# Kernel tuning notes

Hardware: AMD Instinct MI355X
Metric: run time of the kernel (lower is better)

The kernel has to match this reference:

```python
import jax, jax.numpy as jnp
import numpy as np

NUM_HEADS = 16

def setup_inputs() -> dict:
    key = jax.random.key(0)
    ks = jax.random.split(key, 9)
    B, S, D = 8, 1024, 1024
    scale = 1.0 / np.sqrt(D)
    return {
        "query": jax.random.normal(ks[0], (B, S, D), jnp.float32),
        "key": jax.random.normal(ks[1], (B, S, D), jnp.float32),
        "value": jax.random.normal(ks[2], (B, S, D), jnp.float32),
        "Wq": jax.random.normal(ks[3], (D, D), jnp.float32) * scale,
        "bq": jnp.zeros((D,), jnp.float32),
        "Wk": jax.random.normal(ks[4], (D, D), jnp.float32) * scale,
        "bk": jnp.zeros((D,), jnp.float32),
        "Wv": jax.random.normal(ks[5], (D, D), jnp.float32) * scale,
        "bv": jnp.zeros((D,), jnp.float32),
    }

def reference(query, key, value, Wq, bq, Wk, bk, Wv, bv):
    B, S, D = query.shape
    H = NUM_HEADS
    hd = D // H
    def proj(x, W, b):
        # [B, S, D] -> [B, H, S, hd]  (nn.Linear uses x @ W.T + b)
        return (x @ W.T + b).reshape(B, -1, H, hd).transpose(0, 2, 1, 3)
    q = proj(query, Wq, bq)
    k = proj(key, Wk, bk)
    v = proj(value, Wv, bv)
    scores = jnp.einsum('bhqd,bhkd->bhqk', q, k) / (hd ** 0.5)
    w = jax.nn.softmax(scores, axis=-1)
    # relu(tanh(.)) on non-negative softmax probs == tanh, but keep faithful
    w = jax.nn.relu(jnp.tanh(w))
    attn = jnp.einsum('bhqk,bhkd->bhqd', w, v)  # [B, H, Sq, hd]
    attn_output = attn.transpose(0, 2, 1, 3).reshape(B, -1, D)
    attn_output_weights = jnp.mean(w, axis=1)  # [B, Sq, Sk]
    return attn_output, attn_output_weights
```

## Files before the change

### kernel.cpp

```cpp
#include <hip/hip_runtime.h>
#include <hip/hip_bf16.h>

using bf16x8 = __attribute__((ext_vector_type(8))) short;
using f32x4  = __attribute__((ext_vector_type(4))) float;
typedef unsigned short u16;

__device__ __forceinline__ u16 f2bf(float f) {
  unsigned int u = __float_as_uint(f);
  u += 0x7FFFu + ((u >> 16) & 1u);
  return (u16)(u >> 16);
}

__device__ __forceinline__ u16 f2bf_fast(float f) {
  return (u16)((__float_as_uint(f) + 0x8000u) >> 16);
}

__device__ __forceinline__ float bf2f(u16 b) {
  return __uint_as_float(((unsigned int)b) << 16);
}

__device__ __forceinline__ f32x4 mfma16(bf16x8 a, bf16x8 b, f32x4 c) {
  return __builtin_amdgcn_mfma_f32_16x16x32_bf16(a, b, c, 0, 0, 0);
}

__device__ __forceinline__ float tanh2(float p) {
  float x2 = p * p;
  return p * fmaf(x2, -0.33333333f, 1.0f);
}

#define GLL16(gp, lp) __builtin_amdgcn_global_load_lds( \
    (const __attribute__((address_space(1))) unsigned*)(gp), \
    (__attribute__((address_space(3))) unsigned*)(lp), 16, 0, 0)

__global__ __launch_bounds__(256) void cvtX_kernel(
    const float* __restrict__ x0, const float* __restrict__ x1,
    const float* __restrict__ x2, u16* __restrict__ d0,
    u16* __restrict__ d1, u16* __restrict__ d2) {
  const float* src = (blockIdx.y == 0) ? x0 : (blockIdx.y == 1) ? x1 : x2;
  u16* dst = (blockIdx.y == 0) ? d0 : (blockIdx.y == 1) ? d1 : d2;
  const int i = (blockIdx.x * 256 + threadIdx.x) * 8;
  float4 v0 = *reinterpret_cast<const float4*>(src + i);
  float4 v1 = *reinterpret_cast<const float4*>(src + i + 4);
  u16 o[8] = {f2bf(v0.x), f2bf(v0.y), f2bf(v0.z), f2bf(v0.w),
              f2bf(v1.x), f2bf(v1.y), f2bf(v1.z), f2bf(v1.w)};
  *reinterpret_cast<int4*>(dst + i) = *reinterpret_cast<int4*>(o);
}

__global__ __launch_bounds__(256) void cvtW_kernel(
    const float* __restrict__ w0, const float* __restrict__ w1,
    const float* __restrict__ w2, u16* __restrict__ dst) {
  const float* src = (blockIdx.y == 0) ? w0 : (blockIdx.y == 1) ? w1 : w2;
  u16* d = dst + (size_t)blockIdx.y * 1048576;
  const int i = (blockIdx.x * 256 + threadIdx.x) * 8;
  float4 v0 = *reinterpret_cast<const float4*>(src + i);
  float4 v1 = *reinterpret_cast<const float4*>(src + i + 4);
  u16 o[8] = {f2bf(v0.x), f2bf(v0.y), f2bf(v0.z), f2bf(v0.w),
              f2bf(v1.x), f2bf(v1.y), f2bf(v1.z), f2bf(v1.w)};
  *reinterpret_cast<int4*>(d + i) = *reinterpret_cast<int4*>(o);
}

__global__ __launch_bounds__(256) void proj_kernel(
    const u16* __restrict__ Xq, const u16* __restrict__ Xk,
    const u16* __restrict__ Xv, const u16* __restrict__ Wbf,
    const float* __restrict__ Bq, const float* __restrict__ Bk,
    const float* __restrict__ Bv,
    u16* __restrict__ Yq, u16* __restrict__ Yk, u16* __restrict__ Yv)
{
  const int mat = blockIdx.z;
  const u16* X  = (mat == 0) ? Xq : (mat == 1) ? Xk : Xv;
  const u16* W  = Wbf + (size_t)mat * 1048576;
  const float* Bi = (mat == 0) ? Bq : (mat == 1) ? Bk : Bv;
  u16* Y = (mat == 0) ? Yq : (mat == 1) ? Yk : Yv;
  const float scale = (mat == 0) ? 0.125f : 1.0f;

  __shared__ u16 As[2][128][32];
  __shared__ u16 Bs[2][128][32];

  const int tid  = threadIdx.x;
  const int lane = tid & 63;
  const int w    = tid >> 6;
  const int m0 = blockIdx.x * 128;
  const int n0 = blockIdx.y * 128;
  const int wm = (w >> 1) * 64;
  const int wn = (w & 1) * 64;
  const int fr = lane & 15;
  const int fg = lane >> 4;

  const int srow = lane >> 2;
  const int scol = (lane & 3) * 8;
  const u16* agp = X + (size_t)(m0 + w*32 + srow) * 1024 + scol;
  const u16* bgp = W + (size_t)(n0 + w*32 + srow) * 1024 + scol;

  f32x4 zero = {0.f, 0.f, 0.f, 0.f};
  f32x4 acc[4][4];
#pragma unroll
  for (int i = 0; i < 4; i++)
#pragma unroll
    for (int j = 0; j < 4; j++) acc[i][j] = zero;

#define STAGE(buf, kk)                                            \
  do {                                                            \
    GLL16(agp + (kk),            &As[buf][w*32     ][0]);         \
    GLL16(agp + (kk) + 16*1024,  &As[buf][w*32 + 16][0]);         \
    GLL16(bgp + (kk),            &Bs[buf][w*32     ][0]);         \
    GLL16(bgp + (kk) + 16*1024,  &Bs[buf][w*32 + 16][0]);         \
  } while (0)

  STAGE(0, 0);
  __syncthreads();

  int cur = 0;
  for (int kt = 0; kt < 32; kt++) {
    if (kt < 31) STAGE(cur ^ 1, (kt + 1) * 32);

    bf16x8 af[4], bff[4];
#pragma unroll
    for (int i = 0; i < 4; i++) {
      af[i]  = *reinterpret_cast<const bf16x8*>(&As[cur][wm + i*16 + fr][fg*8]);
      bff[i] = *reinterpret_cast<const bf16x8*>(&Bs[cur][wn + i*16 + fr][fg*8]);
    }
#pragma unroll
    for (int i = 0; i < 4; i++)
#pragma unroll
      for (int j = 0; j < 4; j++)
        acc[i][j] = mfma16(af[i], bff[j], acc[i][j]);

    __syncthreads();
    cur ^= 1;
  }
#undef STAGE

#pragma unroll
  for (int j = 0; j < 4; j++) {
    const int n = n0 + wn + j*16 + fr;
    const float bias = Bi[n];
#pragma unroll
    for (int i = 0; i < 4; i++) {
      const int mbase = m0 + wm + i*16 + fg*4;
      if (mat == 2) {
        u16 pk[4];
#pragma unroll
        for (int r = 0; r < 4; r++) pk[r] = f2bf((acc[i][j][r] + bias) * scale);
        const int bidx = mbase >> 10;
        const int s = mbase & 1023;
        *reinterpret_cast<uint2*>(&Y[((size_t)(bidx * 1024 + n)) * 1024 + s]) =
            *reinterpret_cast<uint2*>(pk);
      } else {
#pragma unroll
        for (int r = 0; r < 4; r++) {
          Y[(size_t)(mbase + r) * 1024 + n] = f2bf((acc[i][j][r] + bias) * scale);
        }
      }
    }
  }
}

__global__ __launch_bounds__(256) void attn_out_kernel(
    const u16* __restrict__ Qbf, const u16* __restrict__ Kbf, const u16* __restrict__ Vt,
    float* __restrict__ outA, float* __restrict__ rcpZ)
{
  const int bid = blockIdx.x;
  const int xcd = bid & 7;
  const int wi  = bid >> 3;
  const int qt  = wi & 15;
  const int bh  = ((wi >> 4) << 3) | xcd;
  const int b   = bh >> 4;
  const int h   = bh & 15;

  const int tid  = threadIdx.x;
  const int lane = tid & 63;
  const int w    = tid >> 6;
  const int fr = lane & 15;
  const int fg = lane >> 4;

  __shared__ u16 Ks[2][32][88];
  __shared__ u16 Vts[2][64][40];
  __shared__ u16 Tl[4][16][40];
  __shared__ u16 Tl3[4][16][40];

  const int qbase = qt * 64 + w * 16;

  const u16* qp = Qbf + ((size_t)(b * 1024 + qbase + fr)) * 1024 + h * 64 + fg * 8;
  const bf16x8 qf0 = *reinterpret_cast<const bf16x8*>(qp);
  const bf16x8 qf1 = *reinterpret_cast<const bf16x8*>(qp + 32);

  const int krow = tid >> 3;
  const int koff = (tid & 7) * 8;
  const u16* kp = Kbf + ((size_t)(b * 1024 + krow)) * 1024 + h * 64 + koff;

  const int vrow = tid >> 2;
  const int voff = (tid & 3) * 8;
  const u16* vp = Vt + ((size_t)((b * 16 + h) * 64 + vrow)) * 1024 + voff;

  f32x4 zero = {0.f, 0.f, 0.f, 0.f};
  float zacc[4] = {0.f, 0.f, 0.f, 0.f};
  f32x4 o1[4], o3[4];
#pragma unroll
  for (int e = 0; e < 4; e++) { o1[e] = zero; o3[e] = zero; }

  {
    int4 kv = *reinterpret_cast<const int4*>(kp);
    int4 vv = *reinterpret_cast<const int4*>(vp);
    *reinterpret_cast<int4*>(&Ks[0][krow][koff]) = kv;
    *reinterpret_cast<int4*>(&Vts[0][vrow][voff]) = vv;
  }
  __syncthreads();
  int cur = 0;
  for (int kt = 0; kt < 32; kt++) {
    int4 kvn, vvn;
    if (kt < 31) {
      kvn = *reinterpret_cast<const int4*>(kp + (size_t)(kt + 1) * 32 * 1024);
      vvn = *reinterpret_cast<const int4*>(vp + (kt + 1) * 32);
    }

    bf16x8 k0a = *reinterpret_cast<const bf16x8*>(&Ks[cur][fr][fg*8]);
    bf16x8 k0b = *reinterpret_cast<const bf16x8*>(&Ks[cur][fr][32 + fg*8]);
    bf16x8 k1a = *reinterpret_cast<const bf16x8*>(&Ks[cur][16 + fr][fg*8]);
    bf16x8 k1b = *reinterpret_cast<const bf16x8*>(&Ks[cur][16 + fr][32 + fg*8]);
    f32x4 s0 = zero, s1 = zero;
    s0 = mfma16(qf0, k0a, s0); s0 = mfma16(qf1, k0b, s0);
    s1 = mfma16(qf0, k1a, s1); s1 = mfma16(qf1, k1b, s1);

#pragma unroll
    for (int r = 0; r < 4; r++) {
      float e0 = __expf(s0[r] - 8.f);
      float e1 = __expf(s1[r] - 8.f);
      zacc[r] += e0 + e1;
      Tl[w][fg*4 + r][fr]       = f2bf_fast(e0);
      Tl[w][fg*4 + r][16 + fr]  = f2bf_fast(e1);
      Tl3[w][fg*4 + r][fr]      = f2bf_fast(e0 * e0 * e0);
      Tl3[w][fg*4 + r][16 + fr] = f2bf_fast(e1 * e1 * e1);
    }
    bf16x8 af  = *reinterpret_cast<const bf16x8*>(&Tl[w][fr][fg*8]);
    bf16x8 af3 = *reinterpret_cast<const bf16x8*>(&Tl3[w][fr][fg*8]);
#pragma unroll
    for (int e = 0; e < 4; e++) {
      bf16x8 bv = *reinterpret_cast<const bf16x8*>(&Vts[cur][e*16 + fr][fg*8]);
      o1[e] = mfma16(af,  bv, o1[e]);
      o3[e] = mfma16(af3, bv, o3[e]);
    }

    if (kt < 31) {
      *reinterpret_cast<int4*>(&Ks[cur ^ 1][krow][koff]) = kvn;
      *reinterpret_cast<int4*>(&Vts[cur ^ 1][vrow][voff]) = vvn;
    }
    __syncthreads();
    cur ^= 1;
  }

#pragma unroll
  for (int r = 0; r < 4; r++) {
    float z = zacc[r];
    z += __shfl_xor(z, 1); z += __shfl_xor(z, 2);
    z += __shfl_xor(z, 4); z += __shfl_xor(z, 8);
    zacc[r] = z;
  }
  float rz[4], rz3[4];
#pragma unroll
  for (int r = 0; r < 4; r++) {
    rz[r] = 1.0f / zacc[r];
    rz3[r] = rz[r] * rz[r] * rz[r] * 0.33333333f;
  }
  if (fr == 0) {
#pragma unroll
    for (int r = 0; r < 4; r++)
      rcpZ[((size_t)(b * 16 + h)) * 1024 + qbase + fg * 4 + r] = rz[r];
  }
#pragma unroll
  for (int e = 0; e < 4; e++)
#pragma unroll
    for (int r = 0; r < 4; r++)
      outA[((size_t)(b * 1024 + qbase + fg*4 + r)) * 1024 + h * 64 + e*16 + fr] =
          rz[r] * o1[e][r] - rz3[r] * o3[e][r];
}

__global__ __launch_bounds__(256) void attn_w_kernel(
    const u16* __restrict__ Qbf, const u16* __restrict__ Kbf,
    const float* __restrict__ rcpZ, float* __restrict__ outW)
{
  const int bid = blockIdx.x;
  const int b   = bid & 7;
  const int wi  = bid >> 3;
  const int qt  = wi & 31;
  const int ks  = wi >> 5;
  const int tid  = threadIdx.x;
  const int lane = tid & 63;
  const int w    = tid >> 6;
  const int qi = w >> 1;
  const int ki = w & 1;
  const int fr = lane & 15;
  const int fg = lane >> 4;

  __shared__ u16 Ksh[2][128][72];
  __shared__ float statsL[16][32];

  {
    const int hh = tid >> 5, rr = tid & 31;
    float rzv0 = rcpZ[((size_t)(b * 16 + hh)) * 1024 + qt * 32 + rr];
    statsL[hh][rr] = __logf(rzv0) - 8.f;
    float rzv1 = rcpZ[((size_t)(b * 16 + hh + 8)) * 1024 + qt * 32 + rr];
    statsL[hh + 8][rr] = __logf(rzv1) - 8.f;
  }

  const int srow = tid >> 1;
  const int scol = (tid & 1) * 32;
  const u16* kgp = Kbf + ((size_t)(b * 1024 + ks * 128 + srow)) * 1024 + scol;

  const u16* qp = Qbf + ((size_t)(b * 1024 + qt * 32 + qi * 16 + fr)) * 1024 + fg * 8;

  f32x4 wsum[4];
#pragma unroll
  for (int kt = 0; kt < 4; kt++) wsum[kt] = f32x4{0.f, 0.f, 0.f, 0.f};

  {
#pragma unroll
    for (int j = 0; j < 4; j++)
      *reinterpret_cast<int4*>(&Ksh[0][srow][scol + j*8]) =
          *reinterpret_cast<const int4*>(kgp + j*8);
  }
  __syncthreads();

  int cur = 0;
  for (int h = 0; h < 16; h++) {
    int4 kn[4];
    if (h < 15) {
#pragma unroll
      for (int j = 0; j < 4; j++)
        kn[j] = *reinterpret_cast<const int4*>(kgp + (h + 1) * 64 + j*8);
    }

    bf16x8 a0 = *reinterpret_cast<const bf16x8*>(qp + h * 64);
    bf16x8 a1 = *reinterpret_cast<const bf16x8*>(qp + h * 64 + 32);
    float cl[4];
#pragma unroll
    for (int r = 0; r < 4; r++) cl[r] = statsL[h][qi*16 + fg*4 + r];

#pragma unroll
    for (int kt = 0; kt < 4; kt++) {
      const int krow = ki * 64 + kt * 16 + fr;
      bf16x8 b0 = *reinterpret_cast<const bf16x8*>(&Ksh[cur][krow][fg*8]);
      bf16x8 b1 = *reinterpret_cast<const bf16x8*>(&Ksh[cur][krow][32 + fg*8]);
      f32x4 s = {0.f, 0.f, 0.f, 0.f};
      s = mfma16(a0, b0, s);
      s = mfma16(a1, b1, s);
#pragma unroll
      for (int r = 0; r < 4; r++)
        wsum[kt][r] += tanh2(__expf(s[r] + cl[r]));
    }

    if (h < 15) {
#pragma unroll
      for (int j = 0; j < 4; j++)
        *reinterpret_cast<int4*>(&Ksh[cur ^ 1][srow][scol + j*8]) = kn[j];
    }
    __syncthreads();
    cur ^= 1;
  }

#pragma unroll
  for (int kt = 0; kt < 4; kt++)
#pragma unroll
    for (int r = 0; r < 4; r++)
      outW[((size_t)(b*1024 + qt*32 + qi*16 + fg*4 + r)) * 1024 + ks*128 + ki*64 + kt*16 + fr] =
          wsum[kt][r] * 0.0625f;
}

extern "C" void kernel_launch(void* const* d_in, const int* in_sizes, int n_in,
                              void* d_out, int out_size, void* d_ws, size_t ws_size,
                              hipStream_t stream) {
  const float* query = (const float*)d_in[0];
  const float* key_  = (const float*)d_in[1];
  const float* value = (const float*)d_in[2];
  const float* Wq = (const float*)d_in[3];
  const float* bq = (const float*)d_in[4];
  const float* Wk = (const float*)d_in[5];
  const float* bk = (const float*)d_in[6];
  const float* Wv = (const float*)d_in[7];
  const float* bv = (const float*)d_in[8];

  float* outA = (float*)d_out;
  float* outW = outA + 8388608;

  u16* Qbf = (u16*)d_ws;
  u16* Kbf = Qbf + 8388608;
  u16* Vt  = Kbf + 8388608;
  u16* Xq  = Vt + 8388608;
  u16* Xk  = Xq + 8388608;
  u16* Xv  = Xk + 8388608;
  u16* Wbf = Xv + 8388608;
  float* rcpZ = (float*)(Wbf + 3145728);

  cvtW_kernel<<<dim3(512, 3), 256, 0, stream>>>(Wq, Wk, Wv, Wbf);
  cvtX_kernel<<<dim3(4096, 3), 256, 0, stream>>>(query, key_, value, Xq, Xk, Xv);
  proj_kernel<<<dim3(64, 8, 3), 256, 0, stream>>>(
      Xq, Xk, Xv, Wbf, bq, bk, bv, Qbf, Kbf, Vt);
  attn_out_kernel<<<dim3(2048), dim3(256), 0, stream>>>(Qbf, Kbf, Vt, outA, rcpZ);
  attn_w_kernel<<<dim3(2048), dim3(256), 0, stream>>>(Qbf, Kbf, rcpZ, outW);
}
```

Before: 264.6 us.

## Fold log2e into Q scale, use exp2, halve proj M-tile, compute cubes in registers

```diff
diff --git a/kernel.cpp b/kernel.cpp
--- a/kernel.cpp
+++ b/kernel.cpp
@@ -23,10 +23,15 @@
   return __builtin_amdgcn_mfma_f32_16x16x32_bf16(a, b, c, 0, 0, 0);
 }
 
+#define EXP2F(x) __builtin_amdgcn_exp2f(x)
+#define LOG2F(x) __builtin_amdgcn_logf(x)
+
 __device__ __forceinline__ float tanh2(float p) {
   float x2 = p * p;
   return p * fmaf(x2, -0.33333333f, 1.0f);
 }
+
+#define EXP2_SHIFT 11.54156f
 
 #define GLL16(gp, lp) __builtin_amdgcn_global_load_lds( \
     (const __attribute__((address_space(1))) unsigned*)(gp), \
@@ -71,37 +76,36 @@
   const u16* W  = Wbf + (size_t)mat * 1048576;
   const float* Bi = (mat == 0) ? Bq : (mat == 1) ? Bk : Bv;
   u16* Y = (mat == 0) ? Yq : (mat == 1) ? Yk : Yv;
-  const float scale = (mat == 0) ? 0.125f : 1.0f;
-
-  __shared__ u16 As[2][128][32];
+  const float scale = (mat == 0) ? 0.125f * 1.44269504f : 1.0f;
+
+  __shared__ u16 As[2][64][32];
   __shared__ u16 Bs[2][128][32];
 
   const int tid  = threadIdx.x;
   const int lane = tid & 63;
   const int w    = tid >> 6;
-  const int m0 = blockIdx.x * 128;
+  const int m0 = blockIdx.x * 64;
   const int n0 = blockIdx.y * 128;
-  const int wm = (w >> 1) * 64;
+  const int wm = (w >> 1) * 32;
   const int wn = (w & 1) * 64;
   const int fr = lane & 15;
   const int fg = lane >> 4;
 
   const int srow = lane >> 2;
   const int scol = (lane & 3) * 8;
-  const u16* agp = X + (size_t)(m0 + w*32 + srow) * 1024 + scol;
+  const u16* agp = X + (size_t)(m0 + w*16 + srow) * 1024 + scol;
   const u16* bgp = W + (size_t)(n0 + w*32 + srow) * 1024 + scol;
 
   f32x4 zero = {0.f, 0.f, 0.f, 0.f};
-  f32x4 acc[4][4];
-#pragma unroll
-  for (int i = 0; i < 4; i++)
+  f32x4 acc[2][4];
+#pragma unroll
+  for (int i = 0; i < 2; i++)
 #pragma unroll
     for (int j = 0; j < 4; j++) acc[i][j] = zero;
 
 #define STAGE(buf, kk)                                            \
   do {                                                            \
-    GLL16(agp + (kk),            &As[buf][w*32     ][0]);         \
-    GLL16(agp + (kk) + 16*1024,  &As[buf][w*32 + 16][0]);         \
+    GLL16(agp + (kk),            &As[buf][w*16     ][0]);         \
     GLL16(bgp + (kk),            &Bs[buf][w*32     ][0]);         \
     GLL16(bgp + (kk) + 16*1024,  &Bs[buf][w*32 + 16][0]);         \
   } while (0)
@@ -113,14 +117,15 @@
   for (int kt = 0; kt < 32; kt++) {
     if (kt < 31) STAGE(cur ^ 1, (kt + 1) * 32);
 
-    bf16x8 af[4], bff[4];
-#pragma unroll
-    for (int i = 0; i < 4; i++) {
+    bf16x8 af[2], bff[4];
+#pragma unroll
+    for (int i = 0; i < 2; i++)
       af[i]  = *reinterpret_cast<const bf16x8*>(&As[cur][wm + i*16 + fr][fg*8]);
-      bff[i] = *reinterpret_cast<const bf16x8*>(&Bs[cur][wn + i*16 + fr][fg*8]);
-    }
-#pragma unroll
-    for (int i = 0; i < 4; i++)
+#pragma unroll
+    for (int j = 0; j < 4; j++)
+      bff[j] = *reinterpret_cast<const bf16x8*>(&Bs[cur][wn + j*16 + fr][fg*8]);
+#pragma unroll
+    for (int i = 0; i < 2; i++)
 #pragma unroll
       for (int j = 0; j < 4; j++)
         acc[i][j] = mfma16(af[i], bff[j], acc[i][j]);
@@ -135,7 +140,7 @@
     const int n = n0 + wn + j*16 + fr;
     const float bias = Bi[n];
 #pragma unroll
-    for (int i = 0; i < 4; i++) {
+    for (int i = 0; i < 2; i++) {
       const int mbase = m0 + wm + i*16 + fg*4;
       if (mat == 2) {
         u16 pk[4];
@@ -176,7 +181,6 @@
   __shared__ u16 Ks[2][32][88];
   __shared__ u16 Vts[2][64][40];
   __shared__ u16 Tl[4][16][40];
-  __shared__ u16 Tl3[4][16][40];
 
   const int qbase = qt * 64 + w * 16;
 
@@ -223,16 +227,19 @@
 
 #pragma unroll
     for (int r = 0; r < 4; r++) {
-      float e0 = __expf(s0[r] - 8.f);
-      float e1 = __expf(s1[r] - 8.f);
+      float e0 = EXP2F(s0[r] - EXP2_SHIFT);
+      float e1 = EXP2F(s1[r] - EXP2_SHIFT);
       zacc[r] += e0 + e1;
       Tl[w][fg*4 + r][fr]       = f2bf_fast(e0);
       Tl[w][fg*4 + r][16 + fr]  = f2bf_fast(e1);
-      Tl3[w][fg*4 + r][fr]      = f2bf_fast(e0 * e0 * e0);
-      Tl3[w][fg*4 + r][16 + fr] = f2bf_fast(e1 * e1 * e1);
-    }
-    bf16x8 af  = *reinterpret_cast<const bf16x8*>(&Tl[w][fr][fg*8]);
-    bf16x8 af3 = *reinterpret_cast<const bf16x8*>(&Tl3[w][fr][fg*8]);
+    }
+    bf16x8 af = *reinterpret_cast<const bf16x8*>(&Tl[w][fr][fg*8]);
+    bf16x8 af3;
+#pragma unroll
+    for (int j = 0; j < 8; j++) {
+      float e = bf2f((u16)af[j]);
+      af3[j] = (short)f2bf_fast(e * e * e);
+    }
 #pragma unroll
     for (int e = 0; e < 4; e++) {
       bf16x8 bv = *reinterpret_cast<const bf16x8*>(&Vts[cur][e*16 + fr][fg*8]);
@@ -297,9 +304,9 @@
   {
     const int hh = tid >> 5, rr = tid & 31;
     float rzv0 = rcpZ[((size_t)(b * 16 + hh)) * 1024 + qt * 32 + rr];
-    statsL[hh][rr] = __logf(rzv0) - 8.f;
+    statsL[hh][rr] = LOG2F(rzv0) - EXP2_SHIFT;
     float rzv1 = rcpZ[((size_t)(b * 16 + hh + 8)) * 1024 + qt * 32 + rr];
-    statsL[hh + 8][rr] = __logf(rzv1) - 8.f;
+    statsL[hh + 8][rr] = LOG2F(rzv1) - EXP2_SHIFT;
   }
 
   const int srow = tid >> 1;
@@ -345,7 +352,7 @@
       s = mfma16(a1, b1, s);
 #pragma unroll
       for (int r = 0; r < 4; r++)
-        wsum[kt][r] += tanh2(__expf(s[r] + cl[r]));
+        wsum[kt][r] += tanh2(EXP2F(s[r] + cl[r]));
     }
 
     if (h < 15) {
@@ -392,7 +399,7 @@
 
   cvtW_kernel<<<dim3(512, 3), 256, 0, stream>>>(Wq, Wk, Wv, Wbf);
   cvtX_kernel<<<dim3(4096, 3), 256, 0, stream>>>(query, key_, value, Xq, Xk, Xv);
-  proj_kernel<<<dim3(64, 8, 3), 256, 0, stream>>>(
+  proj_kernel<<<dim3(128, 8, 3), 256, 0, stream>>>(
       Xq, Xk, Xv, Wbf, bq, bk, bv, Qbf, Kbf, Vt);
   attn_out_kernel<<<dim3(2048), dim3(256), 0, stream>>>(Qbf, Kbf, Vt, outA, rcpZ);
   attn_w_kernel<<<dim3(2048), dim3(256), 0, stream>>>(Qbf, Kbf, rcpZ, outW);
```

Result: slower. 271.6 us (+2.7%).
